# Kernel optimization log

Measured on AMD Instinct MI355X. Metric: run time of the kernel, lower is better.

## Reference

```python
import jax, jax.numpy as jnp
import numpy as np

N = 50000      # nodes
E = 800000     # edges
D = 64         # out_feats
L = 5          # n_steps


def setup_inputs() -> dict:
    key = jax.random.key(0)
    ks = jax.random.split(key, 6)
    x = jax.random.normal(ks[0], (N, D), dtype=jnp.float32)
    edge_index = jax.random.randint(ks[1], (2, E), 0, N, dtype=jnp.int64)
    # per-layer message transform weights, uniform(-1/sqrt(D), 1/sqrt(D)) like PyG `uniform`
    bound = 1.0 / np.sqrt(D)
    weight = jax.random.uniform(ks[2], (L, D, D), minval=-bound, maxval=bound, dtype=jnp.float32)
    # GRUCell params (PyTorch layout: [3*D, D] with gate order r, z, n)
    w_ih = jax.random.uniform(ks[3], (3 * D, D), minval=-bound, maxval=bound, dtype=jnp.float32)
    w_hh = jax.random.uniform(ks[4], (3 * D, D), minval=-bound, maxval=bound, dtype=jnp.float32)
    b = jax.random.uniform(ks[5], (2, 3 * D), minval=-bound, maxval=bound, dtype=jnp.float32)
    return {"x": x, "edge_index": edge_index, "weight": weight,
            "w_ih": w_ih, "w_hh": w_hh, "b_ih": b[0], "b_hh": b[1]}


def _gru_cell(m, h, w_ih, w_hh, b_ih, b_hh):
    # PyTorch GRUCell semantics; gate order r, z, n
    gi = m @ w_ih.T + b_ih          # [N, 3D]
    gh = h @ w_hh.T + b_hh          # [N, 3D]
    i_r, i_z, i_n = jnp.split(gi, 3, axis=-1)
    h_r, h_z, h_n = jnp.split(gh, 3, axis=-1)
    r = jax.nn.sigmoid(i_r + h_r)
    z = jax.nn.sigmoid(i_z + h_z)
    n = jnp.tanh(i_n + r * h_n)
    return (1.0 - z) * n + z * h


def reference(x, edge_index, weight, w_ih, w_hh, b_ih, b_hh):
    src, dst = edge_index[0], edge_index[1]  # messages flow src (j) -> dst (i)
    h = x  # input width == out_channels, so padding branch is a no-op
    for i in range(L):
        m = h @ weight[i]                                   # [N, D]
        agg = jax.ops.segment_sum(m[src], dst, num_segments=N)  # scatter-add over edges
        h = _gru_cell(agg, h, w_ih, w_hh, b_ih, b_hh)
    return h
```

## Files before the change

### kernel.cpp

```cpp
#include <hip/hip_runtime.h>
#include <hip/hip_bf16.h>
#include <math.h>

#define DF 64
#define NPB 128
#define EPB 2048
#define DCAP 4608

typedef __attribute__((ext_vector_type(8))) short short8v;
typedef __attribute__((ext_vector_type(4))) float f32x4;

__global__ __launch_bounds__(256) void zero_int_kernel(int* __restrict__ p, int n) {
  int i = blockIdx.x * 256 + threadIdx.x;
  if (i < n) p[i] = 0;
}

__global__ __launch_bounds__(256) void bkt_count_kernel(const int* __restrict__ dst,
                                                        int* __restrict__ bcount,
                                                        int e, int nbk) {
  __shared__ int cnt[512];
  for (int i = threadIdx.x; i < nbk; i += 256) cnt[i] = 0;
  __syncthreads();
  const int eb = blockIdx.x * EPB;
  const int ee = (eb + EPB < e) ? (eb + EPB) : e;
  for (int i = eb + threadIdx.x; i < ee; i += 256) atomicAdd(&cnt[dst[i] >> 7], 1);
  __syncthreads();
  for (int i = threadIdx.x; i < nbk; i += 256)
    if (cnt[i]) atomicAdd(&bcount[i], cnt[i]);
}

__global__ __launch_bounds__(512) void bkt_scan_kernel(const int* __restrict__ bcount,
                                                       int* __restrict__ boff,
                                                       int* __restrict__ bcur,
                                                       int* __restrict__ rowp_last,
                                                       int e, int nbk) {
  __shared__ int a[512];
  const int t = threadIdx.x;
  int v = (t < nbk) ? bcount[t] : 0;
  a[t] = v;
  __syncthreads();
  for (int off = 1; off < 512; off <<= 1) {
    int add = (t >= off) ? a[t - off] : 0;
    __syncthreads();
    a[t] += add;
    __syncthreads();
  }
  int excl = a[t] - v;
  if (t < nbk) { boff[t] = excl; bcur[t] = excl; }
  if (t == nbk - 1) { boff[nbk] = excl + v; rowp_last[0] = e; }
}

__global__ __launch_bounds__(256) void bkt_fill_kernel(const int* __restrict__ src,
                                                       const int* __restrict__ dst,
                                                       int* __restrict__ bcur,
                                                       int2* __restrict__ bpairs,
                                                       int e, int nbk) {
  __shared__ int cnt[512];
  __shared__ int base[512];
  for (int i = threadIdx.x; i < nbk; i += 256) cnt[i] = 0;
  __syncthreads();
  const int eb = blockIdx.x * EPB;
  int s[8], d[8], r[8];
#pragma unroll
  for (int q = 0; q < 8; ++q) {
    int i = eb + q * 256 + threadIdx.x;
    bool ok = i < e;
    s[q] = ok ? src[i] : 0;
    d[q] = ok ? dst[i] : 0;
    r[q] = ok ? atomicAdd(&cnt[d[q] >> 7], 1) : 0;
  }
  __syncthreads();
  for (int i = threadIdx.x; i < nbk; i += 256)
    base[i] = cnt[i] ? atomicAdd(&bcur[i], cnt[i]) : 0;
  __syncthreads();
#pragma unroll
  for (int q = 0; q < 8; ++q) {
    int i = eb + q * 256 + threadIdx.x;
    if (i < e) {
      int b = d[q] >> 7;
      bpairs[base[b] + r[q]] = make_int2(s[q], d[q] & (NPB - 1));
    }
  }
}

__global__ __launch_bounds__(256) void bkt_csr_kernel(const int2* __restrict__ bpairs,
                                                      const int* __restrict__ boff,
                                                      int* __restrict__ rowp,
                                                      int* __restrict__ csr,
                                                      int n, int nbk) {
  __shared__ int cnt[NPB], cur[NPB], sa[NPB];
  __shared__ int lsrc[DCAP], ldst[DCAP], lcsr[DCAP];
  const int b = blockIdx.x;
  const int t = threadIdx.x;
  const int e0 = boff[b];
  int cnt_e = boff[b + 1] - e0;
  if (cnt_e > DCAP) cnt_e = DCAP;
  if (t < NPB) cnt[t] = 0;
  __syncthreads();
  for (int i = t; i < cnt_e; i += 256) {
    int2 p = bpairs[e0 + i];
    lsrc[i] = p.x;
    ldst[i] = p.y;
    atomicAdd(&cnt[p.y], 1);
  }
  __syncthreads();
  if (t < NPB) sa[t] = cnt[t];
  __syncthreads();
  for (int off = 1; off < NPB; off <<= 1) {
    int add = (t < NPB && t >= off) ? sa[t - off] : 0;
    __syncthreads();
    if (t < NPB) sa[t] += add;
    __syncthreads();
  }
  if (t < NPB) {
    int excl = sa[t] - cnt[t];
    cur[t] = excl;
    int node = b * NPB + t;
    if (node < n) rowp[node] = e0 + excl;
  }
  __syncthreads();
  for (int i = t; i < cnt_e; i += 256) {
    int p = atomicAdd(&cur[ldst[i]], 1);
    lcsr[p] = lsrc[i];
  }
  __syncthreads();
  for (int i = t; i < cnt_e; i += 256) csr[e0 + i] = lcsr[i];
}

__global__ __launch_bounds__(256) void wb_kernel(const float* __restrict__ W,
                                                 const float* __restrict__ wih,
                                                 const float* __restrict__ whh,
                                                 __hip_bfloat16* __restrict__ WB,
                                                 int total) {
  int idx = blockIdx.x * 256 + threadIdx.x;
  if (idx >= total) return;
  int k = idx & 127;
  int c = (idx >> 7) & 255;
  int l = idx >> 15;
  int g = c >> 6;
  int f = c & 63;
  float v = 0.f;
  if (k < 64) {
    if (g != 3) {
      int crow = (g == 0) ? f : (g == 1) ? (64 + f) : (128 + f);
      const float* wr = W + ((size_t)l * 64 + k) * 64;
      const float* ir = wih + (size_t)crow * 64;
      float s = 0.f;
#pragma unroll
      for (int t2 = 0; t2 < 64; ++t2) s = fmaf(wr[t2], ir[t2], s);
      v = s;
    }
  } else {
    if (g != 2) {
      int crow = (g == 0) ? f : (g == 1) ? (64 + f) : (128 + f);
      v = whh[(size_t)crow * 64 + (k - 64)];
    }
  }
  WB[idx] = __float2bfloat16(v);
}

__global__ __launch_bounds__(256) void cvt_kernel(const float* __restrict__ x,
                                                  __hip_bfloat16* __restrict__ o, int n) {
  int i = blockIdx.x * 256 + threadIdx.x;
  if (i < n) o[i] = __float2bfloat16(x[i]);
}

__global__ __launch_bounds__(256) void gather_kernel(const __hip_bfloat16* __restrict__ hb,
                                                     const int* __restrict__ rowp,
                                                     const int* __restrict__ csr,
                                                     __hip_bfloat16* __restrict__ segHb,
                                                     int n) {
  int gw = (int)((blockIdx.x * 256 + threadIdx.x) >> 6);
  int lane = threadIdx.x & 63;
  if (gw >= n) return;
  int beg = rowp[gw], end = rowp[gw + 1];
  float acc = 0.f;
  int e = beg;
  for (; e + 4 <= end; e += 4) {
    int s0 = csr[e], s1 = csr[e + 1], s2 = csr[e + 2], s3 = csr[e + 3];
    float v0 = __bfloat162float(hb[(size_t)s0 * DF + lane]);
    float v1 = __bfloat162float(hb[(size_t)s1 * DF + lane]);
    float v2 = __bfloat162float(hb[(size_t)s2 * DF + lane]);
    float v3 = __bfloat162float(hb[(size_t)s3 * DF + lane]);
    acc += v0 + v1 + v2 + v3;
  }
  for (; e < end; ++e) acc += __bfloat162float(hb[(size_t)csr[e] * DF + lane]);
  segHb[(size_t)gw * DF + lane] = __float2bfloat16(acc);
}

__device__ __forceinline__ short8v ldB(const char* sB, int c, int chunk) {
  return *(const short8v*)(sB + c * 256 + ((chunk ^ (c & 15)) * 16));
}

#define MFMA(acc, a, b) acc = __builtin_amdgcn_mfma_f32_16x16x32_bf16(a, b, acc, 0, 0, 0)

__global__ __launch_bounds__(256, 2) void gru_mfma_kernel(
    const __hip_bfloat16* __restrict__ segHb, const float* __restrict__ hin,
    __hip_bfloat16* __restrict__ hbf,
    const float* __restrict__ bih, const float* __restrict__ bhh,
    const __hip_bfloat16* __restrict__ WB, float* __restrict__ hout, int n) {
  __shared__ __hip_bfloat16 sB[256 * 128];
#pragma unroll
  for (int i = 0; i < 16; ++i) {
    int idx = i * 256 + threadIdx.x;
    int c = idx >> 4, ch = idx & 15;
    short8v v = *(const short8v*)(WB + (size_t)c * 128 + ch * 8);
    *(short8v*)((char*)sB + c * 256 + ((ch ^ (c & 15)) * 16)) = v;
  }
  __syncthreads();

  const char* sBc = (const char*)sB;
  const int lane = threadIdx.x & 63;
  const int wid = threadIdx.x >> 6;
  const int row = lane & 15;
  const int quad = lane >> 4;
  const int ch0 = quad, ch1 = 4 + quad, ch2 = 8 + quad, ch3 = 12 + quad;

  float bi_r[4], bi_z[4], bi_n[4], bh_r[4], bh_z[4], bh_n[4];
#pragma unroll
  for (int j = 0; j < 4; ++j) {
    int f = j * 16 + row;
    bi_r[j] = bih[f]; bi_z[j] = bih[64 + f]; bi_n[j] = bih[128 + f];
    bh_r[j] = bhh[f]; bh_z[j] = bhh[64 + f]; bh_n[j] = bhh[128 + f];
  }

  for (int nb0 = blockIdx.x * 64; nb0 < n; nb0 += gridDim.x * 64) {
    const int nb = nb0 + wid * 16;
    if (nb >= n) continue;
    const short8v a0 = *(const short8v*)(segHb + (size_t)(nb + row) * DF + quad * 8);
    const short8v a1 = *(const short8v*)(segHb + (size_t)(nb + row) * DF + 32 + quad * 8);
    const short8v a2 = *(const short8v*)(hbf + (size_t)(nb + row) * DF + quad * 8);
    const short8v a3 = *(const short8v*)(hbf + (size_t)(nb + row) * DF + 32 + quad * 8);

    f32x4 accR[4], accZ[4], accN[4], accH[4];
#pragma unroll
    for (int j = 0; j < 4; ++j) {
      accR[j] = (f32x4){0.f, 0.f, 0.f, 0.f};
      accZ[j] = (f32x4){0.f, 0.f, 0.f, 0.f};
      accN[j] = (f32x4){0.f, 0.f, 0.f, 0.f};
      accH[j] = (f32x4){0.f, 0.f, 0.f, 0.f};
    }
#pragma unroll
    for (int j = 0; j < 4; ++j) {
      MFMA(accR[j], a0, ldB(sBc, j * 16 + row, ch0));
      MFMA(accR[j], a1, ldB(sBc, j * 16 + row, ch1));
      MFMA(accR[j], a2, ldB(sBc, j * 16 + row, ch2));
      MFMA(accR[j], a3, ldB(sBc, j * 16 + row, ch3));
      MFMA(accZ[j], a0, ldB(sBc, 64 + j * 16 + row, ch0));
      MFMA(accZ[j], a1, ldB(sBc, 64 + j * 16 + row, ch1));
      MFMA(accZ[j], a2, ldB(sBc, 64 + j * 16 + row, ch2));
      MFMA(accZ[j], a3, ldB(sBc, 64 + j * 16 + row, ch3));
      MFMA(accN[j], a0, ldB(sBc, 128 + j * 16 + row, ch0));
      MFMA(accN[j], a1, ldB(sBc, 128 + j * 16 + row, ch1));
      MFMA(accH[j], a2, ldB(sBc, 192 + j * 16 + row, ch2));
      MFMA(accH[j], a3, ldB(sBc, 192 + j * 16 + row, ch3));
    }
#pragma unroll
    for (int j = 0; j < 4; ++j) {
#pragma unroll
      for (int e = 0; e < 4; ++e) {
        const int node = nb + quad * 4 + e;
        const int f = j * 16 + row;
        const float hprev = hin[(size_t)node * DF + f];
        const float r = 1.f / (1.f + __expf(-(accR[j][e] + bi_r[j] + bh_r[j])));
        const float z = 1.f / (1.f + __expf(-(accZ[j][e] + bi_z[j] + bh_z[j])));
        const float nn = tanhf(accN[j][e] + bi_n[j] + r * (accH[j][e] + bh_n[j]));
        const float ho = fmaf(z, hprev - nn, nn);
        hout[(size_t)node * DF + f] = ho;
        hbf[(size_t)node * DF + f] = __float2bfloat16(ho);
      }
    }
  }
}

extern "C" void kernel_launch(void* const* d_in, const int* in_sizes, int n_in,
                              void* d_out, int out_size, void* d_ws, size_t ws_size,
                              hipStream_t stream) {
  const float* x   = (const float*)d_in[0];
  const int*   ei  = (const int*)d_in[1];
  const float* wgt = (const float*)d_in[2];
  const float* wih = (const float*)d_in[3];
  const float* whh = (const float*)d_in[4];
  const float* bih = (const float*)d_in[5];
  const float* bhh = (const float*)d_in[6];
  float* out = (float*)d_out;

  const int N = in_sizes[0] / DF;
  const int E = in_sizes[1] / 2;
  const int L = in_sizes[2] / (DF * DF);

  const int* srcv = ei;
  const int* dstv = ei + E;

  float* hA = (float*)d_ws;
  float* hB = hA + (size_t)N * DF;
  __hip_bfloat16* segHb = (__hip_bfloat16*)(hB + (size_t)N * DF);
  __hip_bfloat16* hbf   = segHb + (size_t)N * DF;
  __hip_bfloat16* WB    = hbf + (size_t)N * DF;
  int* rowp   = (int*)(WB + (size_t)L * 256 * 128);
  int* csr    = rowp + (N + 1);
  int* bcount = csr + E;
  int* boff   = bcount + 512;
  int* bcur   = boff + 513;
  int2* bpairs = (int2*)hA;

  const int NBK = (N + NPB - 1) >> 7;
  const int EB  = (E + EPB - 1) / EPB;

  zero_int_kernel<<<(NBK + 255) / 256, 256, 0, stream>>>(bcount, NBK);
  bkt_count_kernel<<<EB, 256, 0, stream>>>(dstv, bcount, E, NBK);
  bkt_scan_kernel<<<1, 512, 0, stream>>>(bcount, boff, bcur, rowp + N, E, NBK);
  bkt_fill_kernel<<<EB, 256, 0, stream>>>(srcv, dstv, bcur, bpairs, E, NBK);
  bkt_csr_kernel<<<NBK, 256, 0, stream>>>(bpairs, boff, rowp, csr, N, NBK);

  wb_kernel<<<(L * 256 * 128 + 255) / 256, 256, 0, stream>>>(wgt, wih, whh, WB,
                                                             L * 256 * 128);
  cvt_kernel<<<(N * DF + 255) / 256, 256, 0, stream>>>(x, hbf, N * DF);

  const float* hin = x;
  const int gruGrid = (N + 63) / 64;
  for (int i = 0; i < L; ++i) {
    gather_kernel<<<(N * DF + 255) / 256, 256, 0, stream>>>(hbf, rowp, csr, segHb, N);
    float* hout = (i == L - 1) ? out : ((i & 1) ? hB : hA);
    gru_mfma_kernel<<<gruGrid, 256, 0, stream>>>(segHb, hin, hbf, bih, bhh,
                                                 WB + (size_t)i * 256 * 128, hout, N);
    hin = hout;
  }
}
```

Before: 369.1 us.

## Vectorize gather over edge groups and drop fp32 hidden-state round trips

The gather kernel now splits each wavefront into four edge groups of 16 lanes, each lane loading four bf16 features as a uint2, and combines the groups with cross-lane shuffles. Each lane therefore issues wider loads and handles more edges at once, instead of a 2-byte load per lane per edge. The GRU kernel now reads the previous hidden state from the bf16 copy rather than an fp32 buffer, and writes fp32 only on the final layer. This removes the fp32 hidden-state reads and writes from intermediate layers, at the cost of precision, since the recurrent h is carried in bf16.

```diff
diff --git a/kernel.cpp b/kernel.cpp
--- a/kernel.cpp
+++ b/kernel.cpp
@@ -170,22 +170,47 @@
                                                      const int* __restrict__ csr,
                                                      __hip_bfloat16* __restrict__ segHb,
                                                      int n) {
-  int gw = (int)((blockIdx.x * 256 + threadIdx.x) >> 6);
-  int lane = threadIdx.x & 63;
-  if (gw >= n) return;
-  int beg = rowp[gw], end = rowp[gw + 1];
-  float acc = 0.f;
-  int e = beg;
-  for (; e + 4 <= end; e += 4) {
-    int s0 = csr[e], s1 = csr[e + 1], s2 = csr[e + 2], s3 = csr[e + 3];
-    float v0 = __bfloat162float(hb[(size_t)s0 * DF + lane]);
-    float v1 = __bfloat162float(hb[(size_t)s1 * DF + lane]);
-    float v2 = __bfloat162float(hb[(size_t)s2 * DF + lane]);
-    float v3 = __bfloat162float(hb[(size_t)s3 * DF + lane]);
-    acc += v0 + v1 + v2 + v3;
-  }
-  for (; e < end; ++e) acc += __bfloat162float(hb[(size_t)csr[e] * DF + lane]);
-  segHb[(size_t)gw * DF + lane] = __float2bfloat16(acc);
+  int w = (int)((blockIdx.x * 256 + threadIdx.x) >> 6);
+  if (w >= n) return;
+  const int lane = threadIdx.x & 63;
+  const int g = lane >> 4;
+  const int fq = lane & 15;
+  const int beg = rowp[w], end = rowp[w + 1];
+  float a0 = 0.f, a1 = 0.f, a2 = 0.f, a3 = 0.f;
+  int e = beg + g;
+  for (; e + 4 < end; e += 8) {
+    int s0 = csr[e], s1 = csr[e + 4];
+    uint2 v0 = *(const uint2*)(hb + (size_t)s0 * DF + fq * 4);
+    uint2 v1 = *(const uint2*)(hb + (size_t)s1 * DF + fq * 4);
+    a0 += __uint_as_float(v0.x << 16);
+    a1 += __uint_as_float(v0.x & 0xffff0000u);
+    a2 += __uint_as_float(v0.y << 16);
+    a3 += __uint_as_float(v0.y & 0xffff0000u);
+    a0 += __uint_as_float(v1.x << 16);
+    a1 += __uint_as_float(v1.x & 0xffff0000u);
+    a2 += __uint_as_float(v1.y << 16);
+    a3 += __uint_as_float(v1.y & 0xffff0000u);
+  }
+  if (e < end) {
+    int s0 = csr[e];
+    uint2 v0 = *(const uint2*)(hb + (size_t)s0 * DF + fq * 4);
+    a0 += __uint_as_float(v0.x << 16);
+    a1 += __uint_as_float(v0.x & 0xffff0000u);
+    a2 += __uint_as_float(v0.y << 16);
+    a3 += __uint_as_float(v0.y & 0xffff0000u);
+  }
+  a0 += __shfl_xor(a0, 16); a1 += __shfl_xor(a1, 16);
+  a2 += __shfl_xor(a2, 16); a3 += __shfl_xor(a3, 16);
+  a0 += __shfl_xor(a0, 32); a1 += __shfl_xor(a1, 32);
+  a2 += __shfl_xor(a2, 32); a3 += __shfl_xor(a3, 32);
+  if (g == 0) {
+    ushort2 p0 = make_ushort2(__bfloat16_as_ushort(__float2bfloat16(a0)),
+                              __bfloat16_as_ushort(__float2bfloat16(a1)));
+    ushort2 p1 = make_ushort2(__bfloat16_as_ushort(__float2bfloat16(a2)),
+                              __bfloat16_as_ushort(__float2bfloat16(a3)));
+    uint2 packed = make_uint2(((uint)p0.y << 16) | p0.x, ((uint)p1.y << 16) | p1.x);
+    *(uint2*)(segHb + (size_t)w * DF + fq * 4) = packed;
+  }
 }
 
 __device__ __forceinline__ short8v ldB(const char* sB, int c, int chunk) {
@@ -195,10 +220,11 @@
 #define MFMA(acc, a, b) acc = __builtin_amdgcn_mfma_f32_16x16x32_bf16(a, b, acc, 0, 0, 0)
 
 __global__ __launch_bounds__(256, 2) void gru_mfma_kernel(
-    const __hip_bfloat16* __restrict__ segHb, const float* __restrict__ hin,
+    const __hip_bfloat16* __restrict__ segHb,
     __hip_bfloat16* __restrict__ hbf,
     const float* __restrict__ bih, const float* __restrict__ bhh,
-    const __hip_bfloat16* __restrict__ WB, float* __restrict__ hout, int n) {
+    const __hip_bfloat16* __restrict__ WB, float* __restrict__ out,
+    int writeOut, int n) {
   __shared__ __hip_bfloat16 sB[256 * 128];
 #pragma unroll
   for (int i = 0; i < 16; ++i) {
@@ -261,13 +287,13 @@
       for (int e = 0; e < 4; ++e) {
         const int node = nb + quad * 4 + e;
         const int f = j * 16 + row;
-        const float hprev = hin[(size_t)node * DF + f];
+        const float hprev = __bfloat162float(hbf[(size_t)node * DF + f]);
         const float r = 1.f / (1.f + __expf(-(accR[j][e] + bi_r[j] + bh_r[j])));
         const float z = 1.f / (1.f + __expf(-(accZ[j][e] + bi_z[j] + bh_z[j])));
         const float nn = tanhf(accN[j][e] + bi_n[j] + r * (accH[j][e] + bh_n[j]));
         const float ho = fmaf(z, hprev - nn, nn);
-        hout[(size_t)node * DF + f] = ho;
         hbf[(size_t)node * DF + f] = __float2bfloat16(ho);
+        if (writeOut) out[(size_t)node * DF + f] = ho;
       }
     }
   }
@@ -292,9 +318,7 @@
   const int* srcv = ei;
   const int* dstv = ei + E;
 
-  float* hA = (float*)d_ws;
-  float* hB = hA + (size_t)N * DF;
-  __hip_bfloat16* segHb = (__hip_bfloat16*)(hB + (size_t)N * DF);
+  __hip_bfloat16* segHb = (__hip_bfloat16*)d_ws;
   __hip_bfloat16* hbf   = segHb + (size_t)N * DF;
   __hip_bfloat16* WB    = hbf + (size_t)N * DF;
   int* rowp   = (int*)(WB + (size_t)L * 256 * 128);
@@ -302,7 +326,7 @@
   int* bcount = csr + E;
   int* boff   = bcount + 512;
   int* bcur   = boff + 513;
-  int2* bpairs = (int2*)hA;
+  int2* bpairs = (int2*)(bcur + 512);
 
   const int NBK = (N + NPB - 1) >> 7;
   const int EB  = (E + EPB - 1) / EPB;
@@ -317,13 +341,11 @@
                                                              L * 256 * 128);
   cvt_kernel<<<(N * DF + 255) / 256, 256, 0, stream>>>(x, hbf, N * DF);
 
-  const float* hin = x;
   const int gruGrid = (N + 63) / 64;
   for (int i = 0; i < L; ++i) {
     gather_kernel<<<(N * DF + 255) / 256, 256, 0, stream>>>(hbf, rowp, csr, segHb, N);
-    float* hout = (i == L - 1) ? out : ((i & 1) ? hB : hA);
-    gru_mfma_kernel<<<gruGrid, 256, 0, stream>>>(segHb, hin, hbf, bih, bhh,
-                                                 WB + (size_t)i * 256 * 128, hout, N);
-    hin = hout;
-  }
-}
+    gru_mfma_kernel<<<gruGrid, 256, 0, stream>>>(segHb, hbf, bih, bhh,
+                                                 WB + (size_t)i * 256 * 128, out,
+                                                 (i == L - 1) ? 1 : 0, N);
+  }
+}
```

Result: faster. 337.9 us (-8.5%).
